# Kernel tuning notes

Hardware: AMD Instinct MI355X
Metric: run time of the kernel (lower is better)

## Reference

```python
import jax, jax.numpy as jnp
import numpy as np

KERNEL_NUM = 4

def _gaussian_kernels(kernel_size, sigmas, centers):
    # sigmas, centers: [4,1] -> kernels [4,K]; matches torch linspace/exp/normalize
    half = (kernel_size - 1) * 0.5
    xs = jnp.linspace(-half, half, kernel_size)  # [K]
    pdf = jnp.exp(-0.5 * ((xs[None, :] - centers) / (sigmas + 0.001)) ** 2)  # [4,K]
    return pdf / (pdf.sum(axis=1, keepdims=True) + 0.01)


def setup_inputs() -> dict:
    key = jax.random.key(0)
    k1, k2, k3, k4 = jax.random.split(key, 4)
    B, C, L = 4, 512, 2048
    return {
        "x": jax.random.normal(k1, (B, C, L), dtype=jnp.float32),
        "q": jax.random.normal(k2, (B, C, L), dtype=jnp.float32),
        "sigmas": jax.random.uniform(k3, (KERNEL_NUM, 1), dtype=jnp.float32),
        "center_shift": jax.random.uniform(k4, (KERNEL_NUM, 1), dtype=jnp.float32),
        "kernel_size": 7,
    }


def reference(x, q, sigmas, center_shift, kernel_size):
    B, C, L = x.shape
    pad = kernel_size // 2
    # --- 4 gaussian blurs as one grouped conv: same kernel for every channel ---
    kern = _gaussian_kernels(kernel_size, sigmas, center_shift)  # [4,K]
    x_pad = jnp.pad(x, ((0, 0), (0, 0), (pad, pad)), mode='edge')  # replicate pad on L
    lhs = x_pad.reshape(B * C, 1, L + 2 * pad)
    rhs = kern[:, None, :]  # [4,1,K] (cross-correlation, like torch conv1d)
    conv = jax.lax.conv_general_dilated(lhs, rhs, (1,), 'VALID',
                                        dimension_numbers=('NCH', 'OIH', 'NCH'))  # [B*C,4,L]
    x_shift = conv.reshape(B, C, KERNEL_NUM, L).transpose(0, 2, 1, 3)  # [B,4,C,L]
    # --- FFT along channel axis (dim=-2), like torch ---
    qf = jnp.fft.fft(q, axis=-2)[:, None]            # [B,1,C,L] complex
    vf = jnp.fft.fft(x_shift, n=C, axis=-2)          # [B,4,C,L] complex
    # --- complex pearson distance over channel axis ---
    mx = vf.mean(axis=-2, keepdims=True)
    my = qf.mean(axis=-2, keepdims=True)
    dx = vf - mx
    dy = qf - my
    cov = dx * dy
    a = (dx ** 2).sum(axis=-2, keepdims=True)
    b = (dy ** 2).sum(axis=-2, keepdims=True)
    rho = cov / jnp.sqrt(a * b + 1e-4)               # complex
    value_imag = jnp.arctan2(rho.imag, rho.real + 1e-4)
    wm = 2.0 / (1.0 + jnp.exp(-value_imag * 0.5)) - 1.0
    wm = jnp.where(jnp.isnan(wm), 0.0, wm)
    wm = jax.lax.stop_gradient(wm)                   # torch: .clone().detach()
    freq_dist = jnp.abs(vf - qf) ** 2
    w = jnp.exp(-freq_dist * 0.5) * wm               # real [B,4,C,L]
    value_filter = qf * (1.0 - w) + vf * w
    outs = jnp.abs(jnp.fft.ifft(value_filter, n=C, axis=-2))  # [B,4,C,L] real
    # --- softmax channel-attention combine over the 4 kernels ---
    qmean = q.mean(axis=-2)                          # [B,L]
    scores = jnp.einsum('bl,bkcl->bck', qmean, outs)  # [B,C,4]
    wa = jax.nn.softmax(scores, axis=-1)
    return jnp.einsum('bck,bkcl->bcl', wa, outs)      # [B,C,L]
```

## Files before the change

### kernel.cpp

```cpp
#include <hip/hip_runtime.h>
#include <hip/hip_bf16.h>

#define B_DIM 4
#define C_DIM 512
#define L_DIM 2048
#define KN 4
#define MAXKS 9

__device__ inline float bf2f(unsigned short u){ return __uint_as_float(((unsigned)u)<<16); }
__device__ inline unsigned short f2bf(float f){
  unsigned u = __float_as_uint(f);
  unsigned r = (u + 0x7fffu + ((u>>16)&1u))>>16;
  return (unsigned short)r;
}

__device__ __forceinline__ float fast_atan2(float y, float x){
  float ax = fabsf(x), ay = fabsf(y);
  float mx = fmaxf(ax, ay), mn = fminf(ax, ay);
  float t = __fdividef(mn, mx);
  float a = t*t;
  float r = t*(0.9998660f + a*(-0.3302995f + a*(0.1801410f + a*(-0.0851330f + a*0.0208351f))));
  r = (ay > ax) ? 1.5707963267948966f - r : r;
  r = (x < 0.f) ? 3.14159265358979323846f - r : r;
  return copysignf(r, y);
}
__device__ __forceinline__ float fast_tanh(float u){
  float e = exp2f(2.8853900817779268f*u);
  return __fdividef(e-1.f, e+1.f);
}

__device__ __forceinline__ void lane_fft_fwd(float* zr, float* zi,
                                             const float* stw_r, const float* stw_i, int lane){
  #pragma unroll
  for (int s=5; s>=0; --s){
    int m = 1<<s;
    bool hi = (lane & m) != 0;
    float wr = stw_r[s], wi = stw_i[s];
    #pragma unroll
    for (int j=0;j<8;++j){
      float pr = __shfl_xor(zr[j], m);
      float pi = __shfl_xor(zi[j], m);
      float sr = hi ? (pr - zr[j]) : (zr[j] + pr);
      float si = hi ? (pi - zi[j]) : (zi[j] + pi);
      float mr = sr*wr - si*wi;
      float mi = sr*wi + si*wr;
      zr[j] = hi ? mr : sr;
      zi[j] = hi ? mi : si;
    }
  }
}

__device__ __forceinline__ void lane_fft_inv(float* zr, float* zi,
                                             const float* stw_r, const float* stw_i, int lane){
  #pragma unroll
  for (int s=0; s<6; ++s){
    int m = 1<<s;
    bool hi = (lane & m) != 0;
    float wr = stw_r[s], wi = -stw_i[s];
    #pragma unroll
    for (int j=0;j<8;++j){
      float pr = __shfl_xor(zr[j], m);
      float pi = __shfl_xor(zi[j], m);
      float ar = hi ? zr[j] : pr;
      float ai = hi ? zi[j] : pi;
      float mr = ar*wr - ai*wi;
      float mi = ar*wi + ai*wr;
      zr[j] = hi ? (pr - mr) : (zr[j] + mr);
      zi[j] = hi ? (pi - mi) : (zi[j] + mi);
    }
  }
}

__device__ __forceinline__ void fft8_reg(float* zr, float* zi, float sgn){
  const float C = 0.70710678118654752f;
  float s0r=zr[0]+zr[4], s0i=zi[0]+zi[4];
  float s1r=zr[0]-zr[4], s1i=zi[0]-zi[4];
  float s2r=zr[2]+zr[6], s2i=zi[2]+zi[6];
  float s3r=zr[2]-zr[6], s3i=zi[2]-zi[6];
  float e0r=s0r+s2r, e0i=s0i+s2i;
  float e2r=s0r-s2r, e2i=s0i-s2i;
  float j3r=-sgn*s3i, j3i=sgn*s3r;
  float e1r=s1r+j3r, e1i=s1i+j3i;
  float e3r=s1r-j3r, e3i=s1i-j3i;
  float t0r=zr[1]+zr[5], t0i=zi[1]+zi[5];
  float t1r=zr[1]-zr[5], t1i=zi[1]-zi[5];
  float t2r=zr[3]+zr[7], t2i=zi[3]+zi[7];
  float t3r=zr[3]-zr[7], t3i=zi[3]-zi[7];
  float o0r=t0r+t2r, o0i=t0i+t2i;
  float o2r=t0r-t2r, o2i=t0i-t2i;
  float k3r=-sgn*t3i, k3i=sgn*t3r;
  float o1r=t1r+k3r, o1i=t1i+k3i;
  float o3r=t1r-k3r, o3i=t1i-k3i;
  float w1o_r = C*o1r - sgn*C*o1i;
  float w1o_i = C*o1i + sgn*C*o1r;
  float w2o_r = -sgn*o2i, w2o_i = sgn*o2r;
  float w3o_r = -C*o3r - sgn*C*o3i;
  float w3o_i = -C*o3i + sgn*C*o3r;
  zr[0]=e0r+o0r;   zi[0]=e0i+o0i;
  zr[4]=e0r-o0r;   zi[4]=e0i-o0i;
  zr[1]=e1r+w1o_r; zi[1]=e1i+w1o_i;
  zr[5]=e1r-w1o_r; zi[5]=e1i-w1o_i;
  zr[2]=e2r+w2o_r; zi[2]=e2i+w2o_i;
  zr[6]=e2r-w2o_r; zi[6]=e2i-w2o_i;
  zr[3]=e3r+w3o_r; zi[3]=e3i+w3o_i;
  zr[7]=e3r-w3o_r; zi[7]=e3i-w3o_i;
}

__device__ __forceinline__ void fft512_fwd(float* zr, float* zi,
    const float* stw_r, const float* stw_i,
    const float* btw_r, const float* btw_i, int lane){
  lane_fft_fwd(zr, zi, stw_r, stw_i, lane);
  #pragma unroll
  for (int j=1;j<8;++j){
    float ar=zr[j], ai=zi[j];
    zr[j]=ar*btw_r[j]-ai*btw_i[j];
    zi[j]=ar*btw_i[j]+ai*btw_r[j];
  }
  fft8_reg(zr, zi, -1.f);
}

__device__ __forceinline__ void fft512_inv(float* zr, float* zi,
    const float* stw_r, const float* stw_i,
    const float* btw_r, const float* btw_i, int lane){
  fft8_reg(zr, zi, +1.f);
  #pragma unroll
  for (int j=1;j<8;++j){
    float ar=zr[j], ai=zi[j];
    zr[j]= ar*btw_r[j]+ai*btw_i[j];
    zi[j]=-ar*btw_i[j]+ai*btw_r[j];
  }
  lane_fft_inv(zr, zi, stw_r, stw_i, lane);
}

__device__ __forceinline__ void rfft_separate(const float* zr, const float* zi,
    float* ar, float* ai, float* br, float* bi, int plane, int lane){
  #pragma unroll
  for (int j=0;j<8;++j){
    const int js = 7-j;
    const int j0 = (8-j)&7;
    float pr = __shfl(zr[js], plane);
    float pi = __shfl(zi[js], plane);
    pr = (lane==0) ? zr[j0] : pr;
    pi = (lane==0) ? zi[j0] : pi;
    ar[j] = 0.5f*(zr[j]+pr);
    ai[j] = 0.5f*(zi[j]-pi);
    br[j] = 0.5f*(zi[j]+pi);
    bi[j] = 0.5f*(pr-zr[j]);
  }
}

__device__ __forceinline__ void wreduce4(float&a,float&b,float&c,float&d){
  #pragma unroll
  for (int off=1; off<64; off<<=1){
    a += __shfl_xor(a,off); b += __shfl_xor(b,off);
    c += __shfl_xor(c,off); d += __shfl_xor(d,off);
  }
}

__device__ __forceinline__ void process_k(float* vr, float* vi,
    const float* qre, const float* qim,
    float myr, float myi, float bsr, float bsi,
    const float* stw_r, const float* stw_i,
    const float* btw_r, const float* btw_i,
    int lane, unsigned short* outp)
{
  float T1r=0.f,T1i=0.f,T2r=0.f,T2i=0.f;
  #pragma unroll
  for (int j=0;j<8;++j){
    T1r += vr[j]; T1i += vi[j];
    T2r += vr[j]*vr[j]-vi[j]*vi[j];
    T2i += 2.f*vr[j]*vi[j];
  }
  wreduce4(T1r,T1i,T2r,T2i);
  float mxr = T1r*(1.f/512.f), mxi = T1i*(1.f/512.f);
  float asr = T2r - (T1r*mxr - T1i*mxi);
  float asi = T2i - (T1r*mxi + T1i*mxr);
  float zr_ = asr*bsr - asi*bsi + 1.0e-4f;
  float zi_ = asr*bsi + asi*bsr;
  float rmag = sqrtf(zr_*zr_+zi_*zi_);
  float dr = sqrtf(fmaxf(0.5f*(rmag+zr_),0.f));
  float di = sqrtf(fmaxf(0.5f*(rmag-zr_),0.f));
  di = (zi_ < 0.f) ? -di : di;
  float den = dr*dr + di*di;
  float invden = __fdividef(1.f, den);
  float invr = (den>0.f) ? dr*invden : 0.f;
  float invi = (den>0.f) ? -di*invden : 0.f;

  #pragma unroll
  for (int j=0;j<8;++j){
    float vr_=vr[j], vi_=vi[j], qr_=qre[j], qi_=qim[j];
    float dxr = vr_-mxr, dxi = vi_-mxi;
    float dyr = qr_-myr, dyi = qi_-myi;
    float cvr = dxr*dyr - dxi*dyi;
    float cvi = dxr*dyi + dxi*dyr;
    float rr = cvr*invr - cvi*invi;
    float ri = cvr*invi + cvi*invr;
    float ang = fast_atan2(ri, rr + 1.0e-4f);
    float wm  = fast_tanh(ang*0.25f);
    if (!(wm==wm)) wm = 0.f;
    float fdr = vr_-qr_, fdi = vi_-qi_;
    float fd2 = fdr*fdr+fdi*fdi;
    float w = exp2f(-0.72134752044448170f*fd2)*wm;
    vr[j] = qr_ + w*fdr;
    vi[j] = qi_ + w*fdi;
  }

  fft512_inv(vr,vi,stw_r,stw_i,btw_r,btw_i,lane);

  unsigned short ob[8];
  #pragma unroll
  for (int j=0;j<8;++j){
    float mag = sqrtf(vr[j]*vr[j]+vi[j]*vi[j])*(1.f/512.f);
    ob[j] = f2bf(mag);
  }
  uint4 pk;
  pk.x = (unsigned)ob[0] | ((unsigned)ob[1]<<16);
  pk.y = (unsigned)ob[2] | ((unsigned)ob[3]<<16);
  pk.z = (unsigned)ob[4] | ((unsigned)ob[5]<<16);
  pk.w = (unsigned)ob[6] | ((unsigned)ob[7]<<16);
  *reinterpret_cast<uint4*>(outp) = pk;
}

__global__ __launch_bounds__(256,3) void col_kernel(
    const float* __restrict__ x, const float* __restrict__ q,
    const float* __restrict__ sigmas, const float* __restrict__ centers,
    const int* __restrict__ ksp,
    unsigned short* __restrict__ outs, float* __restrict__ qmean)
{
  __shared__ float kern[KN][MAXKS];
  int tid  = threadIdx.x;
  int wave = tid >> 6;
  int lane = tid & 63;
  int bid  = blockIdx.x;
  int swz  = (bid & 7)*((B_DIM*L_DIM/4)/8) + (bid >> 3);
  int col  = swz*4 + wave;
  int b = col >> 11;
  int l = col & 2047;
  int ks  = ksp[0];
  int pad = ks >> 1;

  if (tid < KN){
    float half = 0.5f*(float)(ks-1);
    float sg = sigmas[tid] + 0.001f;
    float ce = centers[tid];
    float s = 0.f;
    for (int t=0;t<ks;++t){ float d=((float)t-half-ce)/sg; s += expf(-0.5f*d*d); }
    float inv = 1.f/(s+0.01f);
    for (int t=0;t<ks;++t){ float d=((float)t-half-ce)/sg; kern[tid][t] = expf(-0.5f*d*d)*inv; }
  }

  float qv[8];
  const float* qbase = q + ((size_t)(b*512) + lane*8)*2048 + l;
  #pragma unroll
  for (int j=0;j<8;++j) qv[j] = qbase[(size_t)j*2048];

  const float PI = 3.14159265358979323846f;
  int k1 = (int)(__brev((unsigned)lane) >> 26);
  int plane; { int pk_ = (64-k1)&63; plane = (int)(__brev((unsigned)pk_)>>26); }

  float stw_r[6], stw_i[6];
  #pragma unroll
  for (int s=0; s<6; ++s){
    int m = 1<<s;
    float ang = -PI * (float)(lane & (m-1)) / (float)m;
    stw_r[s]=__cosf(ang); stw_i[s]=__sinf(ang);
  }
  float btw_r[8], btw_i[8];
  #pragma unroll
  for (int j=0;j<8;++j){
    float ang = -2.f*PI*(float)(j*k1)/512.f;
    btw_r[j]=__cosf(ang); btw_i[j]=__sinf(ang);
  }

  __syncthreads();

  float c0[8], c1[8], c2[8], c3[8];
  #pragma unroll
  for (int j=0;j<8;++j){ c0[j]=0.f; c1[j]=0.f; c2[j]=0.f; c3[j]=0.f; }
  const float* xbase = x + ((size_t)(b*512) + lane*8)*2048;
  for (int t=0;t<ks;++t){
    int li = l + t - pad;
    li = li<0 ? 0 : (li>2047 ? 2047 : li);
    float w0=kern[0][t], w1=kern[1][t], w2=kern[2][t], w3=kern[3][t];
    #pragma unroll
    for (int j=0;j<8;++j){
      float xv = xbase[(size_t)j*2048 + li];
      c0[j] += w0*xv; c1[j] += w1*xv; c2[j] += w2*xv; c3[j] += w3*xv;
    }
  }

  fft512_fwd(qv, c0, stw_r,stw_i,btw_r,btw_i, lane);
  float qre[8], qim[8], vr[8], vi[8];
  rfft_separate(qv, c0, qre, qim, vr, vi, plane, lane);

  if (lane==0) qmean[b*2048+l] = qre[0]*(1.f/512.f);

  float S1r=0.f,S1i=0.f,S2r=0.f,S2i=0.f;
  #pragma unroll
  for (int j=0;j<8;++j){
    S1r += qre[j]; S1i += qim[j];
    S2r += qre[j]*qre[j]-qim[j]*qim[j];
    S2i += 2.f*qre[j]*qim[j];
  }
  wreduce4(S1r,S1i,S2r,S2i);
  float myr = S1r*(1.f/512.f), myi = S1i*(1.f/512.f);
  float bsr = S2r - (S1r*myr - S1i*myi);
  float bsi = S2i - (S1r*myi + S1i*myr);

  size_t obase = ((size_t)((b*KN)*2048 + l))*512 + lane*8;
  const size_t kstride = (size_t)2048*512;

  process_k(vr, vi, qre,qim, myr,myi,bsr,bsi, stw_r,stw_i,btw_r,btw_i, lane,
            outs + obase);
  fft512_fwd(c1, c2, stw_r,stw_i,btw_r,btw_i, lane);
  rfft_separate(c1, c2, qv, c0, vr, vi, plane, lane);
  process_k(qv, c0, qre,qim, myr,myi,bsr,bsi, stw_r,stw_i,btw_r,btw_i, lane,
            outs + obase + kstride);
  process_k(vr, vi, qre,qim, myr,myi,bsr,bsi, stw_r,stw_i,btw_r,btw_i, lane,
            outs + obase + 2*kstride);
  #pragma unroll
  for (int j=0;j<8;++j) c2[j]=0.f;
  fft512_fwd(c3, c2, stw_r,stw_i,btw_r,btw_i, lane);
  process_k(c3, c2, qre,qim, myr,myi,bsr,bsi, stw_r,stw_i,btw_r,btw_i, lane,
            outs + obase + 3*kstride);
}

__global__ __launch_bounds__(256) void scores_kernel(
    const unsigned short* __restrict__ outs, const float* __restrict__ qmean,
    float* __restrict__ scores)
{
  int tid = threadIdx.x;
  int l0 = blockIdx.x*128;
  int k = blockIdx.y;
  int b = blockIdx.z;
  int c = tid*2;
  float accx=0.f, accy=0.f;
  for (int l=l0; l<l0+128; ++l){
    float s = qmean[b*2048+l];
    const unsigned short* p = outs + ((size_t)((b*KN+k)*2048 + l))*512 + c;
    unsigned int u = *(const unsigned int*)p;
    accx += s*bf2f((unsigned short)(u&0xffffu));
    accy += s*bf2f((unsigned short)(u>>16));
  }
  atomicAdd(&scores[(size_t)(b*512+c)*KN + k], accx);
  atomicAdd(&scores[(size_t)(b*512+c+1)*KN + k], accy);
}

__global__ __launch_bounds__(256) void combine_kernel(
    const unsigned short* __restrict__ outs, const float* __restrict__ scores,
    float* __restrict__ out)
{
  __shared__ float wa[64][KN];
  int cx = threadIdx.x;
  int ly = threadIdx.y;
  int l0 = blockIdx.x*64;
  int c  = blockIdx.y*64 + cx;
  int b  = blockIdx.z;
  if (ly==0){
    float4 s = *reinterpret_cast<const float4*>(&scores[(size_t)(b*512+c)*KN]);
    float m = fmaxf(fmaxf(s.x,s.y),fmaxf(s.z,s.w));
    float e0=expf(s.x-m), e1=expf(s.y-m), e2=expf(s.z-m), e3=expf(s.w-m);
    float inv = 1.f/(e0+e1+e2+e3);
    wa[cx][0]=e0*inv; wa[cx][1]=e1*inv; wa[cx][2]=e2*inv; wa[cx][3]=e3*inv;
  }
  __syncthreads();
  float acc[16];
  #pragma unroll
  for (int i=0;i<16;++i) acc[i]=0.f;
  for (int k=0;k<KN;++k){
    float w = wa[cx][k];
    const unsigned short* p = outs + ((size_t)((b*KN+k)*2048) + l0 + ly*16)*512 + c;
    #pragma unroll
    for (int i=0;i<16;++i){
      acc[i] += w*bf2f(p[(size_t)i*512]);
    }
  }
  float* op = out + ((size_t)(b*512+c))*2048 + l0 + ly*16;
  #pragma unroll
  for (int i=0;i<16;i+=4){
    float4 v = make_float4(acc[i],acc[i+1],acc[i+2],acc[i+3]);
    *reinterpret_cast<float4*>(op+i) = v;
  }
}

extern "C" void kernel_launch(void* const* d_in, const int* in_sizes, int n_in,
                              void* d_out, int out_size, void* d_ws, size_t ws_size,
                              hipStream_t stream)
{
  const float* x   = (const float*)d_in[0];
  const float* q   = (const float*)d_in[1];
  const float* sig = (const float*)d_in[2];
  const float* cen = (const float*)d_in[3];
  const int*   ksp = (const int*)d_in[4];
  float* out = (float*)d_out;

  unsigned short* outs = (unsigned short*)d_ws;
  size_t outs_elems = (size_t)B_DIM*KN*L_DIM*C_DIM;
  float* qmeanb = (float*)((char*)d_ws + outs_elems*sizeof(unsigned short));
  float* scores = qmeanb + (size_t)B_DIM*L_DIM;

  hipMemsetAsync(scores, 0, (size_t)B_DIM*C_DIM*KN*sizeof(float), stream);

  dim3 g1(B_DIM*L_DIM/4);
  hipLaunchKernelGGL(col_kernel, g1, dim3(256), 0, stream,
                     x, q, sig, cen, ksp, outs, qmeanb);
  dim3 g2(L_DIM/128, KN, B_DIM);
  hipLaunchKernelGGL(scores_kernel, g2, dim3(256), 0, stream, outs, qmeanb, scores);
  dim3 g3(L_DIM/64, C_DIM/64, B_DIM);
  hipLaunchKernelGGL(combine_kernel, g3, dim3(64,4), 0, stream, outs, scores, out);
}
```

Measured before the change: 236.4 us.

## Cut col_kernel register pressure to raise occupancy to eight blocks

Register pressure in col_kernel is reduced so launch bounds can ask for 8 blocks per SM instead of 3. The last two lane-FFT stages use trivial twiddles (±1, ±i) with no stored twiddles. The per-lane inter-stage twiddles are built by repeated complex multiplication from one base twiddle rather than held as 8 precomputed pairs. The q spectrum is spilled to LDS rather than kept in registers, and the output store goes through inline global_store_dwordx4 asm. The risks are spills if the register budget is too tight, extra LDS traffic, and slight twiddle rounding drift from the recurrence.

```diff
diff --git a/kernel.cpp b/kernel.cpp
--- a/kernel.cpp
+++ b/kernel.cpp
@@ -7,11 +7,17 @@
 #define KN 4
 #define MAXKS 9
 
+typedef unsigned int u32x4 __attribute__((ext_vector_type(4)));
+
 __device__ inline float bf2f(unsigned short u){ return __uint_as_float(((unsigned)u)<<16); }
 __device__ inline unsigned short f2bf(float f){
   unsigned u = __float_as_uint(f);
   unsigned r = (u + 0x7fffu + ((u>>16)&1u))>>16;
   return (unsigned short)r;
+}
+
+__device__ __forceinline__ void store16(void* p, u32x4 v){
+  asm volatile("global_store_dwordx4 %0, %1, off" :: "v"(p), "v"(v) : "memory");
 }
 
 __device__ __forceinline__ float fast_atan2(float y, float x){
@@ -32,10 +38,10 @@
 __device__ __forceinline__ void lane_fft_fwd(float* zr, float* zi,
                                              const float* stw_r, const float* stw_i, int lane){
   #pragma unroll
-  for (int s=5; s>=0; --s){
+  for (int s=5; s>=2; --s){
     int m = 1<<s;
     bool hi = (lane & m) != 0;
-    float wr = stw_r[s], wi = stw_i[s];
+    float wr = stw_r[s-2], wi = stw_i[s-2];
     #pragma unroll
     for (int j=0;j<8;++j){
       float pr = __shfl_xor(zr[j], m);
@@ -48,15 +54,65 @@
       zi[j] = hi ? mi : si;
     }
   }
+  {
+    bool hi = (lane & 2) != 0;
+    bool tw = (lane & 3) == 3;
+    #pragma unroll
+    for (int j=0;j<8;++j){
+      float pr = __shfl_xor(zr[j], 2);
+      float pi = __shfl_xor(zi[j], 2);
+      float sr = hi ? (pr - zr[j]) : (zr[j] + pr);
+      float si = hi ? (pi - zi[j]) : (zi[j] + pi);
+      zr[j] = tw ? si : sr;
+      zi[j] = tw ? -sr : si;
+    }
+  }
+  {
+    bool hi = (lane & 1) != 0;
+    #pragma unroll
+    for (int j=0;j<8;++j){
+      float pr = __shfl_xor(zr[j], 1);
+      float pi = __shfl_xor(zi[j], 1);
+      float sr = hi ? (pr - zr[j]) : (zr[j] + pr);
+      float si = hi ? (pi - zi[j]) : (zi[j] + pi);
+      zr[j] = sr; zi[j] = si;
+    }
+  }
 }
 
 __device__ __forceinline__ void lane_fft_inv(float* zr, float* zi,
                                              const float* stw_r, const float* stw_i, int lane){
-  #pragma unroll
-  for (int s=0; s<6; ++s){
+  {
+    bool hi = (lane & 1) != 0;
+    #pragma unroll
+    for (int j=0;j<8;++j){
+      float pr = __shfl_xor(zr[j], 1);
+      float pi = __shfl_xor(zi[j], 1);
+      float sr = hi ? (pr - zr[j]) : (zr[j] + pr);
+      float si = hi ? (pi - zi[j]) : (zi[j] + pi);
+      zr[j] = sr; zi[j] = si;
+    }
+  }
+  {
+    bool hi = (lane & 2) != 0;
+    bool tw = (lane & 1) != 0;
+    #pragma unroll
+    for (int j=0;j<8;++j){
+      float pr = __shfl_xor(zr[j], 2);
+      float pi = __shfl_xor(zi[j], 2);
+      float ar = hi ? zr[j] : pr;
+      float ai = hi ? zi[j] : pi;
+      float mr = tw ? -ai : ar;
+      float mi = tw ?  ar : ai;
+      zr[j] = hi ? (pr - mr) : (zr[j] + mr);
+      zi[j] = hi ? (pi - mi) : (zi[j] + mi);
+    }
+  }
+  #pragma unroll
+  for (int s=2; s<6; ++s){
     int m = 1<<s;
     bool hi = (lane & m) != 0;
-    float wr = stw_r[s], wi = -stw_i[s];
+    float wr = stw_r[s-2], wi = -stw_i[s-2];
     #pragma unroll
     for (int j=0;j<8;++j){
       float pr = __shfl_xor(zr[j], m);
@@ -107,27 +163,30 @@
 }
 
 __device__ __forceinline__ void fft512_fwd(float* zr, float* zi,
-    const float* stw_r, const float* stw_i,
-    const float* btw_r, const float* btw_i, int lane){
+    const float* stw_r, const float* stw_i, float b1r, float b1i, int lane){
   lane_fft_fwd(zr, zi, stw_r, stw_i, lane);
+  float wr = b1r, wi = b1i;
   #pragma unroll
   for (int j=1;j<8;++j){
     float ar=zr[j], ai=zi[j];
-    zr[j]=ar*btw_r[j]-ai*btw_i[j];
-    zi[j]=ar*btw_i[j]+ai*btw_r[j];
+    zr[j]=ar*wr-ai*wi;
+    zi[j]=ar*wi+ai*wr;
+    if (j<7){ float nr = wr*b1r - wi*b1i; wi = wr*b1i + wi*b1r; wr = nr; }
   }
   fft8_reg(zr, zi, -1.f);
 }
 
 __device__ __forceinline__ void fft512_inv(float* zr, float* zi,
-    const float* stw_r, const float* stw_i,
-    const float* btw_r, const float* btw_i, int lane){
+    const float* stw_r, const float* stw_i, float b1r, float b1i, int lane){
   fft8_reg(zr, zi, +1.f);
+  float c1r = b1r, c1i = -b1i;
+  float wr = c1r, wi = c1i;
   #pragma unroll
   for (int j=1;j<8;++j){
     float ar=zr[j], ai=zi[j];
-    zr[j]= ar*btw_r[j]+ai*btw_i[j];
-    zi[j]=-ar*btw_i[j]+ai*btw_r[j];
+    zr[j]=ar*wr-ai*wi;
+    zi[j]=ar*wi+ai*wr;
+    if (j<7){ float nr = wr*c1r - wi*c1i; wi = wr*c1i + wi*c1r; wr = nr; }
   }
   lane_fft_inv(zr, zi, stw_r, stw_i, lane);
 }
@@ -158,10 +217,9 @@
 }
 
 __device__ __forceinline__ void process_k(float* vr, float* vi,
-    const float* qre, const float* qim,
+    const float* qlr, const float* qli,
     float myr, float myi, float bsr, float bsi,
-    const float* stw_r, const float* stw_i,
-    const float* btw_r, const float* btw_i,
+    const float* stw_r, const float* stw_i, float b1r, float b1i,
     int lane, unsigned short* outp)
 {
   float T1r=0.f,T1i=0.f,T2r=0.f,T2i=0.f;
@@ -188,7 +246,8 @@
 
   #pragma unroll
   for (int j=0;j<8;++j){
-    float vr_=vr[j], vi_=vi[j], qr_=qre[j], qi_=qim[j];
+    float qr_ = qlr[j*256], qi_ = qli[j*256];
+    float vr_=vr[j], vi_=vi[j];
     float dxr = vr_-mxr, dxi = vi_-mxi;
     float dyr = qr_-myr, dyi = qi_-myi;
     float cvr = dxr*dyr - dxi*dyi;
@@ -205,7 +264,7 @@
     vi[j] = qi_ + w*fdi;
   }
 
-  fft512_inv(vr,vi,stw_r,stw_i,btw_r,btw_i,lane);
+  fft512_inv(vr,vi,stw_r,stw_i,b1r,b1i,lane);
 
   unsigned short ob[8];
   #pragma unroll
@@ -213,21 +272,24 @@
     float mag = sqrtf(vr[j]*vr[j]+vi[j]*vi[j])*(1.f/512.f);
     ob[j] = f2bf(mag);
   }
-  uint4 pk;
+  u32x4 pk;
   pk.x = (unsigned)ob[0] | ((unsigned)ob[1]<<16);
   pk.y = (unsigned)ob[2] | ((unsigned)ob[3]<<16);
   pk.z = (unsigned)ob[4] | ((unsigned)ob[5]<<16);
   pk.w = (unsigned)ob[6] | ((unsigned)ob[7]<<16);
-  *reinterpret_cast<uint4*>(outp) = pk;
-}
-
-__global__ __launch_bounds__(256,3) void col_kernel(
+  store16(outp, pk);
+}
+
+__global__ __launch_bounds__(256,8) void col_kernel(
     const float* __restrict__ x, const float* __restrict__ q,
     const float* __restrict__ sigmas, const float* __restrict__ centers,
     const int* __restrict__ ksp,
     unsigned short* __restrict__ outs, float* __restrict__ qmean)
 {
   __shared__ float kern[KN][MAXKS];
+  __shared__ float qr_lds[8*4*64];
+  __shared__ float qi_lds[8*4*64];
+
   int tid  = threadIdx.x;
   int wave = tid >> 6;
   int lane = tid & 63;
@@ -258,19 +320,15 @@
   int k1 = (int)(__brev((unsigned)lane) >> 26);
   int plane; { int pk_ = (64-k1)&63; plane = (int)(__brev((unsigned)pk_)>>26); }
 
-  float stw_r[6], stw_i[6];
-  #pragma unroll
-  for (int s=0; s<6; ++s){
+  float stw_r[4], stw_i[4];
+  #pragma unroll
+  for (int s=2; s<6; ++s){
     int m = 1<<s;
     float ang = -PI * (float)(lane & (m-1)) / (float)m;
-    stw_r[s]=__cosf(ang); stw_i[s]=__sinf(ang);
-  }
-  float btw_r[8], btw_i[8];
-  #pragma unroll
-  for (int j=0;j<8;++j){
-    float ang = -2.f*PI*(float)(j*k1)/512.f;
-    btw_r[j]=__cosf(ang); btw_i[j]=__sinf(ang);
-  }
+    stw_r[s-2]=__cosf(ang); stw_i[s-2]=__sinf(ang);
+  }
+  float b1r, b1i;
+  { float ang = -2.f*PI*(float)k1/512.f; b1r=__cosf(ang); b1i=__sinf(ang); }
 
   __syncthreads();
 
@@ -289,7 +347,7 @@
     }
   }
 
-  fft512_fwd(qv, c0, stw_r,stw_i,btw_r,btw_i, lane);
+  fft512_fwd(qv, c0, stw_r,stw_i, b1r,b1i, lane);
   float qre[8], qim[8], vr[8], vi[8];
   rfft_separate(qv, c0, qre, qim, vr, vi, plane, lane);
 
@@ -307,21 +365,26 @@
   float bsr = S2r - (S1r*myr - S1i*myi);
   float bsi = S2i - (S1r*myi + S1i*myr);
 
+  float* qlr = &qr_lds[wave*64 + lane];
+  float* qli = &qi_lds[wave*64 + lane];
+  #pragma unroll
+  for (int j=0;j<8;++j){ qlr[j*256]=qre[j]; qli[j*256]=qim[j]; }
+
   size_t obase = ((size_t)((b*KN)*2048 + l))*512 + lane*8;
   const size_t kstride = (size_t)2048*512;
 
-  process_k(vr, vi, qre,qim, myr,myi,bsr,bsi, stw_r,stw_i,btw_r,btw_i, lane,
+  process_k(vr, vi, qlr,qli, myr,myi,bsr,bsi, stw_r,stw_i,b1r,b1i, lane,
             outs + obase);
-  fft512_fwd(c1, c2, stw_r,stw_i,btw_r,btw_i, lane);
+  fft512_fwd(c1, c2, stw_r,stw_i, b1r,b1i, lane);
   rfft_separate(c1, c2, qv, c0, vr, vi, plane, lane);
-  process_k(qv, c0, qre,qim, myr,myi,bsr,bsi, stw_r,stw_i,btw_r,btw_i, lane,
+  process_k(qv, c0, qlr,qli, myr,myi,bsr,bsi, stw_r,stw_i,b1r,b1i, lane,
             outs + obase + kstride);
-  process_k(vr, vi, qre,qim, myr,myi,bsr,bsi, stw_r,stw_i,btw_r,btw_i, lane,
+  process_k(vr, vi, qlr,qli, myr,myi,bsr,bsi, stw_r,stw_i,b1r,b1i, lane,
             outs + obase + 2*kstride);
   #pragma unroll
-  for (int j=0;j<8;++j) c2[j]=0.f;
-  fft512_fwd(c3, c2, stw_r,stw_i,btw_r,btw_i, lane);
-  process_k(c3, c2, qre,qim, myr,myi,bsr,bsi, stw_r,stw_i,btw_r,btw_i, lane,
+  for (int j=0;j<8;++j) c1[j]=0.f;
+  fft512_fwd(c3, c1, stw_r,stw_i, b1r,b1i, lane);
+  process_k(c3, c1, qlr,qli, myr,myi,bsr,bsi, stw_r,stw_i,b1r,b1i, lane,
             outs + obase + 3*kstride);
 }
 
@@ -399,7 +462,7 @@
   float* qmeanb = (float*)((char*)d_ws + outs_elems*sizeof(unsigned short));
   float* scores = qmeanb + (size_t)B_DIM*L_DIM;
 
-  hipMemsetAsync(scores, 0, (size_t)B_DIM*C_DIM*KN*sizeof(float), stream);
+  (void)hipMemsetAsync(scores, 0, (size_t)B_DIM*C_DIM*KN*sizeof(float), stream);
 
   dim3 g1(B_DIM*L_DIM/4);
   hipLaunchKernelGGL(col_kernel, g1, dim3(256), 0, stream,
```

After: 413.5 us. 1.75x slower.
